# Optimization experiments

Measured on AMD Instinct MI355X. Metric: run time of the kernel, lower is better.

Reference implementation:

```python
import jax, jax.numpy as jnp
import numpy as np

BETA = 0.25
CODEBOOK_SIZE = 4096
DIM = 512


def setup_inputs() -> dict:
    key = jax.random.key(0)
    k1, k2 = jax.random.split(key)
    z_e = jax.random.normal(k1, (16, 1024, 512), dtype=jnp.float32)
    # kaiming_uniform-ish codebook init
    bound = float(np.sqrt(6.0 / ((1.0 + 5.0) * DIM)))
    embed = jax.random.uniform(k2, (CODEBOOK_SIZE, DIM), dtype=jnp.float32,
                               minval=-bound, maxval=bound)
    return {"z_e": z_e, "embed": embed}


def reference(z_e, embed):
    D = embed.shape[1]
    K = embed.shape[0]
    z = z_e.reshape(-1, D)                                   # [N, D]
    N = z.shape[0]
    # squared euclidean distances [N, K]
    distances = (jnp.sum(z * z, axis=1, keepdims=True)
                 - 2.0 * (z @ embed.T)
                 + jnp.sum(embed * embed, axis=1))
    indices = jnp.argmin(distances, axis=1)                  # [N]
    z_q = embed[indices].reshape(z_e.shape)                  # gather == one-hot matmul
    # straight-through estimator
    z_q_st = z_e + jax.lax.stop_gradient(z_q - z_e)
    commitment_loss = jnp.mean((jax.lax.stop_gradient(z_q) - z_e) ** 2)
    vq_loss = BETA * commitment_loss
    # avg_probs = encodings.mean(0) via histogram of indices
    counts = jnp.zeros((K,), dtype=z.dtype).at[indices].add(1.0)
    avg_probs = counts / N
    perplexity = jnp.exp(-jnp.sum(avg_probs * jnp.log(avg_probs + 1e-10)))
    return (z_q_st, indices.reshape(z_e.shape[:-1]), vq_loss, perplexity)
```

## Files before the change

### kernel.cpp

```cpp
#include <hip/hip_runtime.h>
#include <cstdint>
#include <cstddef>

typedef _Float16 f16x8 __attribute__((ext_vector_type(8)));
typedef float f32x4 __attribute__((ext_vector_type(4)));

#define NTOK 16384
#define DIMV 512
#define KCODE 4096

#define IDX_OFF (NTOK * DIMV)
#define LOSSO   (IDX_OFF + NTOK)
#define PERPO   (LOSSO + 1)

static const size_t A2_OFF = 0;
static const size_t B2_OFF = A2_OFF + (size_t)NTOK * DIMV * 2;
static const size_t EN_OFF = B2_OFF + (size_t)KCODE * DIMV * 2;
static const size_t RK_OFF = EN_OFF + (size_t)KCODE * 4;
static const size_t CNT_OFF = RK_OFF + (size_t)NTOK * 32 * 4;
static const size_t RLOSS_OFF = CNT_OFF + (size_t)KCODE * 4;

__device__ __forceinline__ float sqf(float v) {
    float p = v * v;
    asm volatile("" : "+v"(p));
    return p;
}

__device__ __forceinline__ float np_pairwise_sq(const float* xs, int t) {
    float accp = 0.0f;
    if (t < 32) {
        const float* blk = xs + (t >> 3) * 128;
        int j = t & 7;
        float rj = sqf(blk[j]);
#pragma unroll
        for (int tt = 1; tt < 16; ++tt) rj += sqf(blk[tt * 8 + j]);
        accp = rj;
    }
#pragma unroll
    for (int d = 1; d <= 16; d <<= 1) accp += __shfl_xor(accp, d, 64);
    return __shfl(accp, 0, 64);
}

__global__ void prep_z_k(const float* __restrict__ z, _Float16* __restrict__ A2) {
    int t = blockIdx.x * 256 + threadIdx.x;
    int n = t >> 6;
    int dc = (t & 63) << 3;
    const float* zp = z + (size_t)n * DIMV + dc;
    float4 v0 = ((const float4*)zp)[0];
    float4 v1 = ((const float4*)zp)[1];
    float vs[8] = {v0.x, v0.y, v0.z, v0.w, v1.x, v1.y, v1.z, v1.w};
    f16x8 hi;
#pragma unroll
    for (int i = 0; i < 8; ++i) hi[i] = (_Float16)(vs[i] * 256.0f);
    *(f16x8*)(A2 + (size_t)n * DIMV + dc) = hi;
}

__global__ void prep_e_k(const float* __restrict__ e, _Float16* __restrict__ B2,
                         float* __restrict__ C32) {
    __shared__ float es[512];
    int k = blockIdx.x;
    int t = threadIdx.x;
    const float* ep = e + (size_t)k * DIMV + t * 8;
    float4 v0 = ((const float4*)ep)[0];
    float4 v1 = ((const float4*)ep)[1];
    ((float4*)es)[t * 2] = v0;
    ((float4*)es)[t * 2 + 1] = v1;
    float vs[8] = {v0.x, v0.y, v0.z, v0.w, v1.x, v1.y, v1.z, v1.w};
    f16x8 hi;
#pragma unroll
    for (int i = 0; i < 8; ++i) hi[i] = (_Float16)(vs[i] * 256.0f);
    *(f16x8*)(B2 + (size_t)k * DIMV + t * 8) = hi;
    __syncthreads();
    float c = np_pairwise_sq(es, t);
    if (t == 0) C32[k] = c;
}

typedef uint32_t __attribute__((address_space(1))) gas_u32;
typedef uint32_t __attribute__((address_space(3))) las_u32;
__device__ __forceinline__ void g2l16(const _Float16* g, _Float16* l) {
    __builtin_amdgcn_global_load_lds((const gas_u32*)(uintptr_t)g,
                                     (las_u32*)(uint32_t)(uintptr_t)l, 16, 0, 0);
}

__device__ __forceinline__ void top2_merge32(unsigned& k1, unsigned& k2,
                                             unsigned o1, unsigned o2) {
    unsigned n1 = k1 < o1 ? k1 : o1;
    unsigned mx = k1 < o1 ? o1 : k1;
    unsigned n2 = k2 < o2 ? k2 : o2;
    k1 = n1;
    k2 = mx < n2 ? mx : n2;
}

__global__ __launch_bounds__(512) void gemm_top2_k(
    const _Float16* __restrict__ A2, const _Float16* __restrict__ B2,
    const float* __restrict__ C32, unsigned* __restrict__ rk2) {
    __shared__ _Float16 lA[128 * 64];
    __shared__ _Float16 lB[256 * 64];
    const int nt = blockIdx.x;
    const int mt = blockIdx.y;
    const int tid = threadIdx.x;
    const int w = tid >> 6, l = tid & 63;
    const int wm = w & 1, wn = w >> 1;

    const int srow = l >> 3, schunk = l & 7;
    const int gch = (schunk ^ srow) << 3;
    const _Float16* aG = A2 + (size_t)(mt * 128 + w * 16 + srow) * DIMV + gch;
    const _Float16* bG = B2 + (size_t)(nt * 256 + w * 32 + srow) * DIMV + gch;
    _Float16* aL = &lA[(w * 16) * 64];
    _Float16* bL = &lB[(w * 32) * 64];

    const int lane15 = l & 15, q = l >> 4, sx = l & 7;
    const int aRow = (wm * 64 + lane15) * 64;
    const int bRow = (wn * 64 + lane15) * 64;

    f32x4 acc[4][4] = {};

    for (int kt = 0; kt < 8; ++kt) {
        const _Float16* ag = aG + kt * 64;
        const _Float16* bg = bG + kt * 64;
#pragma unroll
        for (int r = 0; r < 2; ++r) g2l16(ag + (size_t)r * 8 * DIMV, aL + r * 512);
#pragma unroll
        for (int r = 0; r < 4; ++r) g2l16(bg + (size_t)r * 8 * DIMV, bL + r * 512);
        __syncthreads();

#pragma unroll
        for (int kk2 = 0; kk2 < 2; ++kk2) {
            f16x8 af[4], bf[4];
            const int ch = ((kk2 * 4 + q) ^ sx) << 3;
#pragma unroll
            for (int i = 0; i < 4; ++i) {
                af[i] = *(const f16x8*)&lA[aRow + i * 1024 + ch];
                bf[i] = *(const f16x8*)&lB[bRow + i * 1024 + ch];
            }
#pragma unroll
            for (int i = 0; i < 4; ++i)
#pragma unroll
                for (int j = 0; j < 4; ++j)
                    acc[i][j] = __builtin_amdgcn_mfma_f32_16x16x32_f16(af[i], bf[j], acc[i][j], 0, 0, 0);
        }
        __syncthreads();
    }

    unsigned* lk32 = (unsigned*)lA;
    const int colL = wn * 64 + lane15;
    float envals[4];
#pragma unroll
    for (int j = 0; j < 4; ++j) envals[j] = C32[nt * 256 + colL + j * 16] * 65536.0f;

#pragma unroll
    for (int i = 0; i < 4; ++i) {
#pragma unroll
        for (int rr = 0; rr < 4; ++rr) {
            unsigned k1 = 0xFFFFFFFFu, k2 = 0xFFFFFFFFu;
#pragma unroll
            for (int j = 0; j < 4; ++j) {
                float dist = envals[j] - 2.0f * acc[i][j][rr];
                unsigned u = __float_as_uint(dist);
                u = (u & 0x80000000u) ? ~u : (u | 0x80000000u);
                unsigned key = (u & 0xFFFFFF00u) | (unsigned)(colL + j * 16);
                if (key < k1) { k2 = k1; k1 = key; } else if (key < k2) k2 = key;
            }
#pragma unroll
            for (int d = 1; d < 16; d <<= 1) {
                unsigned o1 = __shfl_xor(k1, d, 64);
                unsigned o2 = __shfl_xor(k2, d, 64);
                top2_merge32(k1, k2, o1, o2);
            }
            if (lane15 == 0) {
                int rl = wm * 64 + i * 16 + q * 4 + rr;
                lk32[rl * 10 + wn * 2]     = k1;
                lk32[rl * 10 + wn * 2 + 1] = k2;
            }
        }
    }
    __syncthreads();
    if (tid < 128) {
        unsigned a1 = lk32[tid * 10], a2 = lk32[tid * 10 + 1];
#pragma unroll
        for (int p = 1; p < 4; ++p)
            top2_merge32(a1, a2, lk32[tid * 10 + p * 2], lk32[tid * 10 + p * 2 + 1]);
        size_t base = (size_t)(mt * 128 + tid) * 32 + nt * 2;
        rk2[base] = a1;
        rk2[base + 1] = a2;
    }
}

__global__ __launch_bounds__(256) void refine_k(
    const unsigned* __restrict__ rk2,
    const float* __restrict__ embed, const float* __restrict__ z,
    const float* __restrict__ C32,
    float* __restrict__ out, unsigned* __restrict__ counts,
    double* __restrict__ rloss) {
    __shared__ float zs[4][512];
    const int wv = threadIdx.x >> 6, t = threadIdx.x & 63;
    const int r = blockIdx.x * 4 + wv;
    const float4* zp = (const float4*)(z + (size_t)r * DIMV);
    float4 za = zp[t * 2], zb = zp[t * 2 + 1];
    ((float4*)zs[wv])[t * 2] = za;
    ((float4*)zs[wv])[t * 2 + 1] = zb;
    __syncthreads();

    float A32 = np_pairwise_sq(zs[wv], t);

    unsigned long long key = ~0ull;
    if (t < 32) {
        unsigned kraw = rk2[(size_t)r * 32 + t];
        unsigned col = (unsigned)(t >> 1) * 256u + (kraw & 255u);
        key = ((unsigned long long)(kraw & 0xFFFFFF00u) << 32) | col;
    }

    const int g = t >> 3, j = t & 7;
    unsigned mycand = 0;
#pragma unroll
    for (int c = 0; c < 8; ++c) {
        unsigned long long m = key;
#pragma unroll
        for (int d = 1; d < 64; d <<= 1) {
            unsigned long long o = __shfl_xor(m, d, 64);
            m = o < m ? o : m;
        }
        if (c == g) mycand = (unsigned)(m & 0xFFFFFFFFull);
        if (key == m) key = ~0ull;
    }

    const float4* ep = (const float4*)(embed + (size_t)mycand * DIMV);
    double s = 0.0;
#pragma unroll
    for (int it = 0; it < 16; ++it) {
        float4 e4 = ep[j + it * 8];
        float4 z4 = ((const float4*)zs[wv])[j + it * 8];
        s += (double)z4.x * e4.x + (double)z4.y * e4.y +
             (double)z4.z * e4.z + (double)z4.w * e4.w;
    }
#pragma unroll
    for (int d = 1; d < 8; d <<= 1) s += __shfl_xor(s, d, 64);

    float Bf = (float)s;
    float d32 = (A32 - 2.0f * Bf) + C32[mycand];
    unsigned u = __float_as_uint(d32);
    u = (u & 0x80000000u) ? ~u : (u | 0x80000000u);
    unsigned long long dk = ((unsigned long long)u << 32) | mycand;
#pragma unroll
    for (int d = 8; d < 64; d <<= 1) {
        unsigned long long o = __shfl_xor(dk, d, 64);
        dk = o < dk ? o : dk;
    }
    const unsigned ibest = (unsigned)(dk & 0xFFFFFFFFull);

    const float4* wp = (const float4*)(embed + (size_t)ibest * DIMV);
    float4 wa = wp[t * 2], wb = wp[t * 2 + 1];
    float4* op = (float4*)(out + (size_t)r * DIMV);
    op[t * 2] = wa;
    op[t * 2 + 1] = wb;
    double dx0 = (double)za.x - wa.x, dx1 = (double)za.y - wa.y;
    double dx2 = (double)za.z - wa.z, dx3 = (double)za.w - wa.w;
    double dx4 = (double)zb.x - wb.x, dx5 = (double)zb.y - wb.y;
    double dx6 = (double)zb.z - wb.z, dx7 = (double)zb.w - wb.w;
    double ls = dx0 * dx0 + dx1 * dx1 + dx2 * dx2 + dx3 * dx3 +
                dx4 * dx4 + dx5 * dx5 + dx6 * dx6 + dx7 * dx7;
#pragma unroll
    for (int d = 1; d < 64; d <<= 1) ls += __shfl_xor(ls, d, 64);
    if (t == 0) {
        out[IDX_OFF + r] = (float)ibest;
        rloss[r] = ls;
        atomicAdd(&counts[ibest], 1u);
    }
}

__global__ void scalars_k(const unsigned* __restrict__ counts,
                          const double* __restrict__ rloss, float* __restrict__ out) {
    int t = threadIdx.x;
    double ls = 0.0;
    for (int i = t; i < NTOK; i += 256) ls += rloss[i];
#pragma unroll
    for (int d = 1; d < 64; d <<= 1) ls += __shfl_xor(ls, d, 64);
    float s = 0.0f;
    for (int i = t; i < KCODE; i += 256) {
        float p = (float)counts[i] * (1.0f / (float)NTOK);
        s += p * logf(p + 1e-10f);
    }
#pragma unroll
    for (int d = 1; d < 64; d <<= 1) s += __shfl_xor(s, d, 64);
    __shared__ float red[4];
    __shared__ double redd[4];
    if ((t & 63) == 0) { red[t >> 6] = s; redd[t >> 6] = ls; }
    __syncthreads();
    if (t == 0) {
        float tot = red[0] + red[1] + red[2] + red[3];
        double ltot = redd[0] + redd[1] + redd[2] + redd[3];
        out[PERPO] = expf(-tot);
        out[LOSSO] = 0.25f * (float)(ltot * (1.0 / (double)(NTOK * DIMV)));
    }
}

extern "C" void kernel_launch(void* const* d_in, const int* in_sizes, int n_in,
                              void* d_out, int out_size, void* d_ws, size_t ws_size,
                              hipStream_t stream) {
    const float* z     = (const float*)d_in[0];
    const float* embed = (const float*)d_in[1];
    float* out = (float*)d_out;
    char* ws = (char*)d_ws;

    _Float16* A2 = (_Float16*)(ws + A2_OFF);
    _Float16* B2 = (_Float16*)(ws + B2_OFF);
    float* C32 = (float*)(ws + EN_OFF);
    unsigned* rk2 = (unsigned*)(ws + RK_OFF);
    unsigned* counts = (unsigned*)(ws + CNT_OFF);
    double* rloss = (double*)(ws + RLOSS_OFF);

    hipMemsetAsync(counts, 0, (size_t)KCODE * 4, stream);

    prep_z_k<<<4096, 256, 0, stream>>>(z, A2);
    prep_e_k<<<KCODE, 64, 0, stream>>>(embed, B2, C32);
    gemm_top2_k<<<dim3(16, 128), 512, 0, stream>>>(A2, B2, C32, rk2);
    refine_k<<<NTOK / 4, 256, 0, stream>>>(rk2, embed, z, C32, out, counts, rloss);
    scalars_k<<<1, 256, 0, stream>>>(counts, rloss, out);
}
```

Before: 253.6 us.

## Fuse prep kernels and memset, use DPP top-2 reduction, shrink refine candidates

Merges the z and codebook conversion kernels and the counts memset into one launch, cutting launch overhead. In the GEMM epilogue the float-to-ordered-uint flip is replaced by adding a positive bias, so raw float bits sort correctly, and the shuffle top-2 reduction becomes DPP row shifts. The refine stage now rescores 4 candidates per row instead of 8, giving 16 lanes per candidate. Rescoring fewer candidates lowers refinement cost but makes wrong argmin choices more likely when fp16 distances are close, and the bias assumes distances stay positive and below a fixed range.

Measured after the change: 221.7 us. 12.6% less time.

```diff
diff --git a/kernel.cpp b/kernel.cpp
--- a/kernel.cpp
+++ b/kernel.cpp
@@ -41,38 +41,40 @@
     return __shfl(accp, 0, 64);
 }
 
-__global__ void prep_z_k(const float* __restrict__ z, _Float16* __restrict__ A2) {
-    int t = blockIdx.x * 256 + threadIdx.x;
-    int n = t >> 6;
-    int dc = (t & 63) << 3;
-    const float* zp = z + (size_t)n * DIMV + dc;
-    float4 v0 = ((const float4*)zp)[0];
-    float4 v1 = ((const float4*)zp)[1];
-    float vs[8] = {v0.x, v0.y, v0.z, v0.w, v1.x, v1.y, v1.z, v1.w};
-    f16x8 hi;
-#pragma unroll
-    for (int i = 0; i < 8; ++i) hi[i] = (_Float16)(vs[i] * 256.0f);
-    *(f16x8*)(A2 + (size_t)n * DIMV + dc) = hi;
-}
-
-__global__ void prep_e_k(const float* __restrict__ e, _Float16* __restrict__ B2,
-                         float* __restrict__ C32) {
-    __shared__ float es[512];
-    int k = blockIdx.x;
-    int t = threadIdx.x;
-    const float* ep = e + (size_t)k * DIMV + t * 8;
-    float4 v0 = ((const float4*)ep)[0];
-    float4 v1 = ((const float4*)ep)[1];
-    ((float4*)es)[t * 2] = v0;
-    ((float4*)es)[t * 2 + 1] = v1;
-    float vs[8] = {v0.x, v0.y, v0.z, v0.w, v1.x, v1.y, v1.z, v1.w};
-    f16x8 hi;
-#pragma unroll
-    for (int i = 0; i < 8; ++i) hi[i] = (_Float16)(vs[i] * 256.0f);
-    *(f16x8*)(B2 + (size_t)k * DIMV + t * 8) = hi;
-    __syncthreads();
-    float c = np_pairwise_sq(es, t);
-    if (t == 0) C32[k] = c;
+__global__ void prep_k(const float* __restrict__ z, const float* __restrict__ e,
+                       _Float16* __restrict__ A2, _Float16* __restrict__ B2,
+                       float* __restrict__ C32, unsigned* __restrict__ counts) {
+    __shared__ float es[4][512];
+    const int b = blockIdx.x;
+    if (b < 4096) {
+        int t = b * 256 + threadIdx.x;
+        int n = t >> 6;
+        int dc = (t & 63) << 3;
+        const float* zp = z + (size_t)n * DIMV + dc;
+        float4 v0 = ((const float4*)zp)[0];
+        float4 v1 = ((const float4*)zp)[1];
+        float vs[8] = {v0.x, v0.y, v0.z, v0.w, v1.x, v1.y, v1.z, v1.w};
+        f16x8 hi;
+#pragma unroll
+        for (int i = 0; i < 8; ++i) hi[i] = (_Float16)(vs[i] * 256.0f);
+        *(f16x8*)(A2 + (size_t)n * DIMV + dc) = hi;
+    } else {
+        const int wv = threadIdx.x >> 6, t = threadIdx.x & 63;
+        const int k = (b - 4096) * 4 + wv;
+        const float* ep = e + (size_t)k * DIMV + t * 8;
+        float4 v0 = ((const float4*)ep)[0];
+        float4 v1 = ((const float4*)ep)[1];
+        ((float4*)es[wv])[t * 2] = v0;
+        ((float4*)es[wv])[t * 2 + 1] = v1;
+        float vs[8] = {v0.x, v0.y, v0.z, v0.w, v1.x, v1.y, v1.z, v1.w};
+        f16x8 hi;
+#pragma unroll
+        for (int i = 0; i < 8; ++i) hi[i] = (_Float16)(vs[i] * 256.0f);
+        *(f16x8*)(B2 + (size_t)k * DIMV + t * 8) = hi;
+        float c = np_pairwise_sq(es[wv], t);
+        if (t == 0) C32[k] = c;
+        if (threadIdx.x < 4) counts[(b - 4096) * 4 + threadIdx.x] = 0u;
+    }
 }
 
 typedef uint32_t __attribute__((address_space(1))) gas_u32;
@@ -90,6 +92,13 @@
     k1 = n1;
     k2 = mx < n2 ? mx : n2;
 }
+
+#define DPP_TOP2(CTRL)                                                                     \
+    {                                                                                      \
+        unsigned o1 = (unsigned)__builtin_amdgcn_update_dpp(-1, (int)k1, CTRL, 0xF, 0xF, false); \
+        unsigned o2 = (unsigned)__builtin_amdgcn_update_dpp(-1, (int)k2, CTRL, 0xF, 0xF, false); \
+        top2_merge32(k1, k2, o1, o2);                                                      \
+    }
 
 __global__ __launch_bounds__(512) void gemm_top2_k(
     const _Float16* __restrict__ A2, const _Float16* __restrict__ B2,
@@ -146,7 +155,7 @@
     const int colL = wn * 64 + lane15;
     float envals[4];
 #pragma unroll
-    for (int j = 0; j < 4; ++j) envals[j] = C32[nt * 256 + colL + j * 16] * 65536.0f;
+    for (int j = 0; j < 4; ++j) envals[j] = C32[nt * 256 + colL + j * 16] * 65536.0f + 4.0e6f;
 
 #pragma unroll
     for (int i = 0; i < 4; ++i) {
@@ -156,18 +165,14 @@
 #pragma unroll
             for (int j = 0; j < 4; ++j) {
                 float dist = envals[j] - 2.0f * acc[i][j][rr];
-                unsigned u = __float_as_uint(dist);
-                u = (u & 0x80000000u) ? ~u : (u | 0x80000000u);
-                unsigned key = (u & 0xFFFFFF00u) | (unsigned)(colL + j * 16);
+                unsigned key = (__float_as_uint(dist) & 0xFFFFFF00u) | (unsigned)(colL + j * 16);
                 if (key < k1) { k2 = k1; k1 = key; } else if (key < k2) k2 = key;
             }
-#pragma unroll
-            for (int d = 1; d < 16; d <<= 1) {
-                unsigned o1 = __shfl_xor(k1, d, 64);
-                unsigned o2 = __shfl_xor(k2, d, 64);
-                top2_merge32(k1, k2, o1, o2);
-            }
-            if (lane15 == 0) {
+            DPP_TOP2(0x118)
+            DPP_TOP2(0x114)
+            DPP_TOP2(0x112)
+            DPP_TOP2(0x111)
+            if (lane15 == 15) {
                 int rl = wm * 64 + i * 16 + q * 4 + rr;
                 lk32[rl * 10 + wn * 2]     = k1;
                 lk32[rl * 10 + wn * 2 + 1] = k2;
@@ -210,10 +215,10 @@
         key = ((unsigned long long)(kraw & 0xFFFFFF00u) << 32) | col;
     }
 
-    const int g = t >> 3, j = t & 7;
+    const int g = t >> 4, j = t & 15;
     unsigned mycand = 0;
 #pragma unroll
-    for (int c = 0; c < 8; ++c) {
+    for (int c = 0; c < 4; ++c) {
         unsigned long long m = key;
 #pragma unroll
         for (int d = 1; d < 64; d <<= 1) {
@@ -227,14 +232,14 @@
     const float4* ep = (const float4*)(embed + (size_t)mycand * DIMV);
     double s = 0.0;
 #pragma unroll
-    for (int it = 0; it < 16; ++it) {
-        float4 e4 = ep[j + it * 8];
-        float4 z4 = ((const float4*)zs[wv])[j + it * 8];
+    for (int it = 0; it < 8; ++it) {
+        float4 e4 = ep[j + it * 16];
+        float4 z4 = ((const float4*)zs[wv])[j + it * 16];
         s += (double)z4.x * e4.x + (double)z4.y * e4.y +
              (double)z4.z * e4.z + (double)z4.w * e4.w;
     }
 #pragma unroll
-    for (int d = 1; d < 8; d <<= 1) s += __shfl_xor(s, d, 64);
+    for (int d = 1; d < 16; d <<= 1) s += __shfl_xor(s, d, 64);
 
     float Bf = (float)s;
     float d32 = (A32 - 2.0f * Bf) + C32[mycand];
@@ -242,7 +247,7 @@
     u = (u & 0x80000000u) ? ~u : (u | 0x80000000u);
     unsigned long long dk = ((unsigned long long)u << 32) | mycand;
 #pragma unroll
-    for (int d = 8; d < 64; d <<= 1) {
+    for (int d = 16; d < 64; d <<= 1) {
         unsigned long long o = __shfl_xor(dk, d, 64);
         dk = o < dk ? o : dk;
     }
@@ -309,10 +314,7 @@
     unsigned* counts = (unsigned*)(ws + CNT_OFF);
     double* rloss = (double*)(ws + RLOSS_OFF);
 
-    hipMemsetAsync(counts, 0, (size_t)KCODE * 4, stream);
-
-    prep_z_k<<<4096, 256, 0, stream>>>(z, A2);
-    prep_e_k<<<KCODE, 64, 0, stream>>>(embed, B2, C32);
+    prep_k<<<5120, 256, 0, stream>>>(z, embed, A2, B2, C32, counts);
     gemm_top2_k<<<dim3(16, 128), 512, 0, stream>>>(A2, B2, C32, rk2);
     refine_k<<<NTOK / 4, 256, 0, stream>>>(rk2, embed, z, C32, out, counts, rloss);
     scalars_k<<<1, 256, 0, stream>>>(counts, rloss, out);
```
